# Performance work log

Measured on AMD Instinct MI355X. Metric: run time of the kernel, lower is better.

Reference implementation:

```python
import jax, jax.numpy as jnp
import numpy as np

DIM = 768
HEADS = 12
HEAD_DIM = DIM // HEADS
MAX_LEN = 2048
EPS = 1e-5

def layer_norm(x, w, b):
    mu = jnp.mean(x, axis=-1, keepdims=True)
    var = jnp.var(x, axis=-1, keepdims=True)
    return (x - mu) * jax.lax.rsqrt(var + EPS) * w + b


def setup_inputs() -> dict:
    key = jax.random.key(0)
    ks = jax.random.split(key, 16)
    B, N = 2, 2048
    s = 1.0 / np.sqrt(DIM)
    inp = {
        "visible_features": jax.random.normal(ks[0], (B, N, DIM), jnp.float32),
        "infrared_features": jax.random.normal(ks[1], (B, N, DIM), jnp.float32),
        "wq": jax.random.normal(ks[2], (DIM, DIM), jnp.float32) * s,
        "bq": jnp.zeros((DIM,), jnp.float32),
        "lnq_w": jnp.ones((DIM,), jnp.float32),
        "lnq_b": jnp.zeros((DIM,), jnp.float32),
        "wk": jax.random.normal(ks[3], (DIM, DIM), jnp.float32) * s,
        "bk": jnp.zeros((DIM,), jnp.float32),
        "lnk_w": jnp.ones((DIM,), jnp.float32),
        "lnk_b": jnp.zeros((DIM,), jnp.float32),
        "wv": jax.random.normal(ks[4], (DIM, DIM), jnp.float32) * s,
        "bv": jnp.zeros((DIM,), jnp.float32),
        "lnv_w": jnp.ones((DIM,), jnp.float32),
        "lnv_b": jnp.zeros((DIM,), jnp.float32),
        "pos_emb": jax.random.normal(ks[5], (MAX_LEN, DIM), jnp.float32),
        "wo": jax.random.normal(ks[6], (DIM, DIM), jnp.float32) * s,
        "bo": jnp.zeros((DIM,), jnp.float32),
        "gate_w": jax.random.normal(ks[7], (DIM, 2 * DIM), jnp.float32) * (1.0 / np.sqrt(2 * DIM)),
        "gate_b": jnp.zeros((DIM,), jnp.float32),
        "ln_w": jnp.ones((DIM,), jnp.float32),
        "ln_b": jnp.zeros((DIM,), jnp.float32),
    }
    return inp


def reference(visible_features, infrared_features, wq, bq, lnq_w, lnq_b,
              wk, bk, lnk_w, lnk_b, wv, bv, lnv_w, lnv_b,
              pos_emb, wo, bo, gate_w, gate_b, ln_w, ln_b):
    B, N, _ = visible_features.shape
    scale = HEAD_DIM ** -0.5

    def proj_heads(x, w, b, gw, gb):
        y = layer_norm(x @ w.T + b, gw, gb)  # [B,N,D]
        return y.reshape(B, N, HEADS, HEAD_DIM).transpose(0, 2, 1, 3)  # [B,H,N,d]

    q = proj_heads(infrared_features, wq, bq, lnq_w, lnq_b)
    k = proj_heads(visible_features, wk, bk, lnk_w, lnk_b)
    v = proj_heads(visible_features, wv, bv, lnv_w, lnv_b)

    pos = pos_emb[:N].reshape(1, N, HEADS, HEAD_DIM).transpose(0, 2, 1, 3)  # [1,H,N,d]

    scores = jnp.einsum('bhnd,bhmd->bhnm', q, k) * scale
    scores = scores + jnp.einsum('bhnd,xhmd->bhnm', q, pos)
    attn = jax.nn.softmax(scores, axis=-1)  # dropout is identity in eval

    out = jnp.einsum('bhnm,bhmd->bhnd', attn, v)
    out = out.transpose(0, 2, 1, 3).reshape(B, N, DIM)
    out = out @ wo.T + bo

    gate = jax.nn.sigmoid(jnp.concatenate([visible_features, out], axis=-1) @ gate_w.T + gate_b)
    fused = visible_features * gate + out * (1.0 - gate)
    return layer_norm(fused, ln_w, ln_b)
```

## Files before the change

### kernel.cpp

```cpp
#include <hip/hip_runtime.h>
#include <hip/hip_bf16.h>

#define DIMC 768
#define NSEQ 2048
#define NB 2
#define NH 12
#define HD 64
#define EPSLN 1e-5f
#define LOG2E 1.44269504f

typedef __attribute__((ext_vector_type(8))) short          bf16x8;
typedef __attribute__((ext_vector_type(8))) unsigned short ushort8;
typedef __attribute__((ext_vector_type(4))) unsigned short ushort4v;
typedef __attribute__((ext_vector_type(4))) float          f32x4;
typedef unsigned int u32;

__device__ __forceinline__ unsigned short f2b(float f) {
    union { float f; unsigned u; } x; x.f = f;
    unsigned r = x.u + 0x7fffu + ((x.u >> 16) & 1u);
    return (unsigned short)(r >> 16);
}
__device__ __forceinline__ float b2f(unsigned short v) {
    union { unsigned u; float f; } x; x.u = ((u32)v) << 16; return x.f;
}

#define MFMA16(a, b, c) __builtin_amdgcn_mfma_f32_16x16x32_bf16((a), (b), (c), 0, 0, 0)

__device__ __forceinline__ void gl_lds16(const unsigned short* g, unsigned short* l) {
    __builtin_amdgcn_global_load_lds(
        (const __attribute__((address_space(1))) u32*)(const void*)g,
        (__attribute__((address_space(3))) u32*)(void*)l, 16, 0, 0);
}

#define G_WQ   147456
#define G_MW   442368
#define G_G2   147456
#define G_WO   147456
#define G_VIS  786432
#define G_INF  786432
#define G_BF_TOTAL (G_WQ + G_MW + G_G2 + G_WO + G_VIS + G_INF)
#define G_BIAS 576
#define G_ALL  (G_BF_TOTAL + G_BIAS)

__global__ __launch_bounds__(256)
void cast_all_kernel(const float* __restrict__ wq, const float* __restrict__ wk,
                     const float* __restrict__ wv, const float* __restrict__ gw,
                     const float* __restrict__ wo,
                     const float* __restrict__ bk, const float* __restrict__ bv,
                     const float* __restrict__ gb,
                     const float* __restrict__ vis, const float* __restrict__ inf_,
                     unsigned short* __restrict__ o_wq, unsigned short* __restrict__ o_mw,
                     unsigned short* __restrict__ o_g2, unsigned short* __restrict__ o_wo,
                     unsigned short* __restrict__ o_vis, unsigned short* __restrict__ o_inf,
                     float* __restrict__ o_biasc)
{
    const int g = blockIdx.x * 256 + threadIdx.x;
    if (g >= G_ALL) return;
    if (g >= G_BF_TOTAL) {
        const int e0 = (g - G_BF_TOTAL) * 4;
        float4 r;
        float* pr = (float*)&r;
        #pragma unroll
        for (int t = 0; t < 4; ++t) {
            const int e = e0 + t;
            pr[t] = (e < 768) ? bk[e] : (e < 1536) ? bv[e - 768] : gb[e - 1536];
        }
        *(float4*)&o_biasc[e0] = r;
        return;
    }
    const float* src; unsigned short* dst; int soff, doff = 0;
    int gg = g;
    if (gg < G_WQ) { src = wq; dst = o_wq; soff = gg; doff = gg; }
    else if ((gg -= G_WQ) < G_MW) {
        const int row = gg / 192, c4 = gg % 192;
        dst = o_mw; doff = gg;
        if      (row < 768)  { src = wk; soff = row * 192 + c4; }
        else if (row < 1536) { src = wv; soff = (row - 768) * 192 + c4; }
        else                 { src = gw; soff = (row - 1536) * 384 + c4; }
    }
    else if ((gg -= G_MW) < G_G2) {
        const int row = gg / 192, c4 = gg % 192;
        src = gw; soff = row * 384 + 192 + c4; dst = o_g2; doff = gg;
    }
    else if ((gg -= G_G2) < G_WO)  { src = wo;   dst = o_wo;  soff = gg; doff = gg; }
    else if ((gg -= G_WO) < G_VIS) { src = vis;  dst = o_vis; soff = gg; doff = gg; }
    else { gg -= G_VIS;              src = inf_; dst = o_inf; soff = gg; doff = gg; }
    f32x4 v = ((const f32x4*)src)[soff];
    ushort4v t;
    t[0] = f2b(v[0]); t[1] = f2b(v[1]); t[2] = f2b(v[2]); t[3] = f2b(v[3]);
    ((ushort4v*)dst)[doff] = t;
}

template<int MODE>
__global__ __launch_bounds__(256)
void gemm128(const unsigned short* __restrict__ A,
             const unsigned short* __restrict__ W,
             const float* __restrict__ bias,
             float* __restrict__ Cf,
             unsigned short* __restrict__ Cb)
{
    __shared__ unsigned short As[128 * 64];
    __shared__ unsigned short Bs[128 * 64];
    const int m0 = blockIdx.x * 128, n0 = blockIdx.y * 128;
    const int lane = threadIdx.x & 63, wid = threadIdx.x >> 6;
    const int wm = wid >> 1, wn = wid & 1;
    const int r16 = lane & 15, kg = lane >> 4;
    const int lrow = lane >> 3;
    const int lcol = (lane & 7) * 8;

    f32x4 acc[4][4] = {};

    for (int k0 = 0; k0 < DIMC; k0 += 64) {
        if (k0) __syncthreads();
        #pragma unroll
        for (int i = 0; i < 4; ++i) {
            const int c = wid * 4 + i;
            const int row = c * 8 + lrow;
            gl_lds16(&A[(size_t)(m0 + row) * DIMC + k0 + lcol], &As[c * 512]);
            gl_lds16(&W[(size_t)(n0 + row) * DIMC + k0 + lcol], &Bs[c * 512]);
        }
        __syncthreads();
        #pragma unroll
        for (int ks = 0; ks < 2; ++ks) {
            bf16x8 af[4], bg[4];
            #pragma unroll
            for (int mi = 0; mi < 4; ++mi)
                af[mi] = *(const bf16x8*)&As[(wm * 64 + mi * 16 + r16) * 64 + ks * 32 + kg * 8];
            #pragma unroll
            for (int nj = 0; nj < 4; ++nj)
                bg[nj] = *(const bf16x8*)&Bs[(wn * 64 + nj * 16 + r16) * 64 + ks * 32 + kg * 8];
            __builtin_amdgcn_s_setprio(1);
            #pragma unroll
            for (int mi = 0; mi < 4; ++mi)
                #pragma unroll
                for (int nj = 0; nj < 4; ++nj)
                    acc[mi][nj] = MFMA16(af[mi], bg[nj], acc[mi][nj]);
            __builtin_amdgcn_s_setprio(0);
        }
    }

    #pragma unroll
    for (int mi = 0; mi < 4; ++mi)
    #pragma unroll
    for (int nj = 0; nj < 4; ++nj) {
        const int gr = m0 + wm * 64 + mi * 16 + kg * 4;
        const int gc = n0 + wn * 64 + nj * 16 + r16;
        const float bvl = (MODE == 3) ? 0.f : bias[gc];
        #pragma unroll
        for (int r = 0; r < 4; ++r) {
            const float val = acc[mi][nj][r] + bvl;
            if (MODE == 0) {
                Cf[(size_t)(gr + r) * DIMC + gc] = val;
            } else if (MODE == 1) {
                if (gc < 1536) Cb[(size_t)(gr + r) * 1536 + gc] = f2b(val);
                else           Cf[(size_t)(gr + r) * DIMC + (gc - 1536)] = val;
            } else if (MODE == 2) {
                const size_t idx = (size_t)(gr + r) * DIMC + gc;
                Cf[idx] = val;
                Cb[idx] = f2b(val);
            } else {
                const size_t idx = (size_t)(gr + r) * DIMC + gc;
                Cf[idx] += val;
            }
        }
    }
}

template<int INBF, int MODE>
__global__ __launch_bounds__(256)
void ln_bf16_kernel(const void* __restrict__ Zv,
                    int ld,
                    const float* __restrict__ w,
                    const float* __restrict__ b,
                    const float* __restrict__ pos,
                    unsigned short* __restrict__ out)
{
    const int row = blockIdx.x;
    const int n = row & (NSEQ - 1);
    float x[3];
    float s = 0.f, q = 0.f;
    #pragma unroll
    for (int u = 0; u < 3; ++u) {
        const int j = threadIdx.x + u * 256;
        if (INBF) x[u] = b2f(((const unsigned short*)Zv)[(size_t)row * ld + j]);
        else      x[u] = ((const float*)Zv)[(size_t)row * ld + j];
        s += x[u];
        q += x[u] * x[u];
    }
    #pragma unroll
    for (int off = 32; off > 0; off >>= 1) {
        s += __shfl_down(s, off);
        q += __shfl_down(q, off);
    }
    __shared__ float ls[8];
    const int wv_ = threadIdx.x >> 6;
    if ((threadIdx.x & 63) == 0) { ls[wv_] = s; ls[4 + wv_] = q; }
    __syncthreads();
    if (threadIdx.x == 0) {
        ls[0] = ls[0] + ls[1] + ls[2] + ls[3];
        ls[4] = ls[4] + ls[5] + ls[6] + ls[7];
    }
    __syncthreads();
    const float mu  = ls[0] * (1.f / DIMC);
    const float var = ls[4] * (1.f / DIMC) - mu * mu;
    const float rs  = rsqrtf(var + EPSLN);
    #pragma unroll
    for (int u = 0; u < 3; ++u) {
        const int j = threadIdx.x + u * 256;
        float y = (x[u] - mu) * rs * w[j] + b[j];
        if (MODE == 1) y = y * (0.125f * LOG2E) + pos[(size_t)n * DIMC + j] * LOG2E;
        out[(size_t)row * DIMC + j] = f2b(y);
    }
}

__global__ __launch_bounds__(256)
void attn_bf16_kernel(const unsigned short* __restrict__ Q,
                      const unsigned short* __restrict__ K,
                      const unsigned short* __restrict__ V,
                      unsigned short* __restrict__ O)
{
    __shared__ unsigned short Ks[64][72];
    __shared__ unsigned short Vt[64][72];
    __shared__ unsigned short Ps[4][16][72];

    const int bh = blockIdx.x;
    const int b = bh / NH, h = bh % NH;
    const int n0 = blockIdx.y * 64;
    const int lane = threadIdx.x & 63, w = threadIdx.x >> 6;
    const int r16 = lane & 15, kg = lane >> 4;

    const size_t base = (size_t)b * NSEQ * DIMC + (size_t)h * HD;

    const size_t qoff = base + (size_t)(n0 + w * 16 + r16) * DIMC + kg * 8;
    bf16x8 aq0 = *(const bf16x8*)&Q[qoff];
    bf16x8 aq1 = *(const bf16x8*)&Q[qoff + 32];

    f32x4 o[4] = {};
    float m_run = -1e30f, l_run = 0.f;

    for (int m0 = 0; m0 < NSEQ; m0 += 64) {
        __syncthreads();
        {
            const int kv = threadIdx.x >> 2;
            const int c  = (threadIdx.x & 3) * 16;
            const size_t go = base + (size_t)(m0 + kv) * DIMC + c;
            *(ushort8*)&Ks[kv][c]     = *(const ushort8*)&K[go];
            *(ushort8*)&Ks[kv][c + 8] = *(const ushort8*)&K[go + 8];
        }
        {
            const int kv = threadIdx.x & 63;
            const int dg = (threadIdx.x >> 6) * 16;
            const size_t go = base + (size_t)(m0 + kv) * DIMC + dg;
            #pragma unroll
            for (int i = 0; i < 4; ++i) {
                ushort4v v4 = *(const ushort4v*)&V[go + i * 4];
                Vt[dg + i * 4 + 0][kv] = v4[0];
                Vt[dg + i * 4 + 1][kv] = v4[1];
                Vt[dg + i * 4 + 2][kv] = v4[2];
                Vt[dg + i * 4 + 3][kv] = v4[3];
            }
        }
        __syncthreads();

        f32x4 sv[4];
        #pragma unroll
        for (int f = 0; f < 4; ++f) sv[f] = (f32x4){0.f, 0.f, 0.f, 0.f};
        __builtin_amdgcn_s_setprio(1);
        #pragma unroll
        for (int f = 0; f < 4; ++f) {
            bf16x8 kb0 = *(const bf16x8*)&Ks[f * 16 + r16][kg * 8];
            bf16x8 kb1 = *(const bf16x8*)&Ks[f * 16 + r16][32 + kg * 8];
            sv[f] = MFMA16(kb0, aq0, sv[f]);
            sv[f] = MFMA16(kb1, aq1, sv[f]);
        }
        __builtin_amdgcn_s_setprio(0);

        float mt = sv[0][0];
        #pragma unroll
        for (int f = 0; f < 4; ++f)
            #pragma unroll
            for (int j = 0; j < 4; ++j)
                mt = fmaxf(mt, sv[f][j]);
        mt = fmaxf(mt, __shfl_xor(mt, 16));
        mt = fmaxf(mt, __shfl_xor(mt, 32));
        const float mnew = fmaxf(m_run, mt);
        const float corr = exp2f(m_run - mnew);
        float p[4][4];
        float st = 0.f;
        #pragma unroll
        for (int f = 0; f < 4; ++f)
            #pragma unroll
            for (int j = 0; j < 4; ++j) {
                p[f][j] = exp2f(sv[f][j] - mnew);
                st += p[f][j];
            }
        st += __shfl_xor(st, 16);
        st += __shfl_xor(st, 32);
        l_run = l_run * corr + st;
        m_run = mnew;

        #pragma unroll
        for (int f = 0; f < 4; ++f) {
            u32 w0, w1;
            asm("v_cvt_pk_bf16_f32 %0, %1, %2" : "=v"(w0) : "v"(p[f][0]), "v"(p[f][1]));
            asm("v_cvt_pk_bf16_f32 %0, %1, %2" : "=v"(w1) : "v"(p[f][2]), "v"(p[f][3]));
            *(u32*)&Ps[w][r16][kg * 4 + 16 * f]     = w0;
            *(u32*)&Ps[w][r16][kg * 4 + 2 + 16 * f] = w1;
        }

        #pragma unroll
        for (int jj = 0; jj < 4; ++jj) {
            const float cq = __shfl(corr, kg * 4 + jj);
            o[0][jj] *= cq; o[1][jj] *= cq; o[2][jj] *= cq; o[3][jj] *= cq;
        }

        bf16x8 pa0 = *(const bf16x8*)&Ps[w][r16][kg * 8];
        bf16x8 pa1 = *(const bf16x8*)&Ps[w][r16][32 + kg * 8];
        __builtin_amdgcn_s_setprio(1);
        #pragma unroll
        for (int nj = 0; nj < 4; ++nj) {
            bf16x8 vb0 = *(const bf16x8*)&Vt[nj * 16 + r16][kg * 8];
            bf16x8 vb1 = *(const bf16x8*)&Vt[nj * 16 + r16][32 + kg * 8];
            o[nj] = MFMA16(pa0, vb0, o[nj]);
            o[nj] = MFMA16(pa1, vb1, o[nj]);
        }
        __builtin_amdgcn_s_setprio(0);
    }

    float linv[4];
    #pragma unroll
    for (int jj = 0; jj < 4; ++jj)
        linv[jj] = 1.f / __shfl(l_run, kg * 4 + jj);
    #pragma unroll
    for (int nj = 0; nj < 4; ++nj)
    #pragma unroll
    for (int jj = 0; jj < 4; ++jj) {
        const size_t go = base + (size_t)(n0 + w * 16 + kg * 4 + jj) * DIMC + nj * 16 + r16;
        O[go] = f2b(o[nj][jj] * linv[jj]);
    }
}

__global__ __launch_bounds__(256)
void fuse_ln_kernel(const float* __restrict__ vis,
                    const float* __restrict__ Oc,
                    const float* __restrict__ G,
                    const float* __restrict__ w,
                    const float* __restrict__ b,
                    float* __restrict__ out)
{
    const int row = blockIdx.x;
    float f[3];
    float s = 0.f, q = 0.f;
    #pragma unroll
    for (int u = 0; u < 3; ++u) {
        const size_t idx = (size_t)row * DIMC + threadIdx.x + u * 256;
        const float vv = vis[idx];
        const float oo = Oc[idx];
        const float gg = 1.f / (1.f + __expf(-G[idx]));
        f[u] = vv * gg + oo * (1.f - gg);
        s += f[u];
        q += f[u] * f[u];
    }
    #pragma unroll
    for (int off = 32; off > 0; off >>= 1) {
        s += __shfl_down(s, off);
        q += __shfl_down(q, off);
    }
    __shared__ float ls[8];
    const int wv_ = threadIdx.x >> 6;
    if ((threadIdx.x & 63) == 0) { ls[wv_] = s; ls[4 + wv_] = q; }
    __syncthreads();
    if (threadIdx.x == 0) {
        ls[0] = ls[0] + ls[1] + ls[2] + ls[3];
        ls[4] = ls[4] + ls[5] + ls[6] + ls[7];
    }
    __syncthreads();
    const float mu  = ls[0] * (1.f / DIMC);
    const float var = ls[4] * (1.f / DIMC) - mu * mu;
    const float rs  = rsqrtf(var + EPSLN);
    #pragma unroll
    for (int u = 0; u < 3; ++u) {
        const int j = threadIdx.x + u * 256;
        out[(size_t)row * DIMC + j] = (f[u] - mu) * rs * w[j] + b[j];
    }
}

extern "C" void kernel_launch(void* const* d_in, const int* in_sizes, int n_in,
                              void* d_out, int out_size, void* d_ws, size_t ws_size,
                              hipStream_t stream)
{
    const float* vis  = (const float*)d_in[0];
    const float* inf_ = (const float*)d_in[1];
    const float* wq   = (const float*)d_in[2];
    const float* bq   = (const float*)d_in[3];
    const float* lnqw = (const float*)d_in[4];
    const float* lnqb = (const float*)d_in[5];
    const float* wk   = (const float*)d_in[6];
    const float* bk   = (const float*)d_in[7];
    const float* lnkw = (const float*)d_in[8];
    const float* lnkb = (const float*)d_in[9];
    const float* wv   = (const float*)d_in[10];
    const float* bv   = (const float*)d_in[11];
    const float* lnvw = (const float*)d_in[12];
    const float* lnvb = (const float*)d_in[13];
    const float* pos  = (const float*)d_in[14];
    const float* wo   = (const float*)d_in[15];
    const float* bo   = (const float*)d_in[16];
    const float* gw   = (const float*)d_in[17];
    const float* gb   = (const float*)d_in[18];
    const float* lnw  = (const float*)d_in[19];
    const float* lnb  = (const float*)d_in[20];

    const size_t WEL = 589824;
    const size_t MWEL = 1769472;
    const size_t BUF = (size_t)NB * NSEQ * DIMC;

    unsigned short* p = (unsigned short*)d_ws;
    unsigned short* wq_b  = p;  p += WEL;
    unsigned short* mw_b  = p;  p += MWEL;
    unsigned short* g2_b  = p;  p += WEL;
    unsigned short* wo_b  = p;  p += WEL;
    unsigned short* vis_b = p;  p += BUF;
    unsigned short* inf_b = p;  p += BUF;
    unsigned short* q_b   = p;  p += BUF;
    unsigned short* k_b   = p;  p += BUF;
    unsigned short* v_b   = p;  p += BUF;
    unsigned short* kvpre = p;  p += 2 * BUF;
    float* biasc = (float*)p;

    float* Gd  = (float*)d_out;
    float* Oc  = (float*)k_b;
    unsigned short* oc_b = inf_b;

    dim3 blk(256);

    cast_all_kernel<<<dim3((G_ALL + 255) / 256), blk, 0, stream>>>(
        wq, wk, wv, gw, wo, bk, bv, gb, vis, inf_,
        wq_b, mw_b, g2_b, wo_b, vis_b, inf_b, biasc);

    gemm128<0><<<dim3(32, 6), blk, 0, stream>>>(inf_b, wq_b, bq, Gd, nullptr);
    ln_bf16_kernel<0, 0><<<dim3(4096), blk, 0, stream>>>(Gd, DIMC, lnqw, lnqb, nullptr, q_b);

    gemm128<1><<<dim3(32, 18), blk, 0, stream>>>(vis_b, mw_b, biasc, Gd, kvpre);
    ln_bf16_kernel<1, 1><<<dim3(4096), blk, 0, stream>>>(kvpre, 1536, lnkw, lnkb, pos, k_b);
    ln_bf16_kernel<1, 0><<<dim3(4096), blk, 0, stream>>>(kvpre + DIMC, 1536, lnvw, lnvb, nullptr, v_b);

    attn_bf16_kernel<<<dim3(NB * NH, NSEQ / 64), blk, 0, stream>>>(q_b, k_b, v_b, q_b);

    gemm128<2><<<dim3(32, 6), blk, 0, stream>>>(q_b, wo_b, bo, Oc, oc_b);

    gemm128<3><<<dim3(32, 6), blk, 0, stream>>>(oc_b, g2_b, nullptr, Gd, nullptr);

    fuse_ln_kernel<<<dim3(4096), blk, 0, stream>>>(vis, Oc, Gd, lnw, lnb, (float*)d_out);
}
```

Measured before the change: 326.1 us.

## Double-buffer GEMM tiles, prefetch K/V and defer softmax rescaling in attention

The GEMM kernel moves to 128x64 output tiles with double-buffered LDS staging and explicit vmcnt waits, so global loads overlap the MFMA work and more blocks are launched. The attention kernel now handles 128 query rows per block (32 per wave), which reuses each K/V tile over twice as many queries. It also prefetches the next K/V tile into registers during compute, and skips the running-max update and output rescale while the max grows by at most 8 in log2 units. The tradeoffs are more registers and LDS per block, only 384 attention blocks (fewer than before, which may hurt occupancy), and larger unnormalised exponentials under deferred rescaling.

```diff
diff --git a/kernel.cpp b/kernel.cpp
--- a/kernel.cpp
+++ b/kernel.cpp
@@ -93,58 +93,73 @@
 
 template<int MODE>
 __global__ __launch_bounds__(256)
-void gemm128(const unsigned short* __restrict__ A,
-             const unsigned short* __restrict__ W,
-             const float* __restrict__ bias,
-             float* __restrict__ Cf,
-             unsigned short* __restrict__ Cb)
+void gemm128x64(const unsigned short* __restrict__ A,
+                const unsigned short* __restrict__ W,
+                const float* __restrict__ bias,
+                float* __restrict__ Cf,
+                unsigned short* __restrict__ Cb)
 {
-    __shared__ unsigned short As[128 * 64];
-    __shared__ unsigned short Bs[128 * 64];
-    const int m0 = blockIdx.x * 128, n0 = blockIdx.y * 128;
+    __shared__ unsigned short As[2][128 * 64];
+    __shared__ unsigned short Bs[2][64 * 64];
+    const int m0 = blockIdx.x * 128, n0 = blockIdx.y * 64;
     const int lane = threadIdx.x & 63, wid = threadIdx.x >> 6;
     const int wm = wid >> 1, wn = wid & 1;
     const int r16 = lane & 15, kg = lane >> 4;
-    const int lrow = lane >> 3;
-    const int lcol = (lane & 7) * 8;
-
-    f32x4 acc[4][4] = {};
-
-    for (int k0 = 0; k0 < DIMC; k0 += 64) {
-        if (k0) __syncthreads();
+    const int lr = lane >> 3, lc = (lane & 7) * 8;
+
+    f32x4 acc[4][2] = {};
+
+    auto stage = [&](int k0, int buf) {
         #pragma unroll
         for (int i = 0; i < 4; ++i) {
             const int c = wid * 4 + i;
-            const int row = c * 8 + lrow;
-            gl_lds16(&A[(size_t)(m0 + row) * DIMC + k0 + lcol], &As[c * 512]);
-            gl_lds16(&W[(size_t)(n0 + row) * DIMC + k0 + lcol], &Bs[c * 512]);
-        }
-        __syncthreads();
+            gl_lds16(&A[(size_t)(m0 + c * 8 + lr) * DIMC + k0 + lc], &As[buf][c * 512]);
+        }
+        #pragma unroll
+        for (int i = 0; i < 2; ++i) {
+            const int c = wid * 2 + i;
+            gl_lds16(&W[(size_t)(n0 + c * 8 + lr) * DIMC + k0 + lc], &Bs[buf][c * 512]);
+        }
+    };
+
+    stage(0, 0);
+    for (int t = 0; t < 12; ++t) {
+        const int cur = t & 1;
+        if (t < 11) {
+            stage((t + 1) * 64, cur ^ 1);
+            asm volatile("s_waitcnt vmcnt(6)" ::: "memory");
+        } else {
+            asm volatile("s_waitcnt vmcnt(0)" ::: "memory");
+        }
+        __builtin_amdgcn_s_barrier();
+        __builtin_amdgcn_sched_barrier(0);
         #pragma unroll
         for (int ks = 0; ks < 2; ++ks) {
-            bf16x8 af[4], bg[4];
+            bf16x8 af[4], bg[2];
             #pragma unroll
             for (int mi = 0; mi < 4; ++mi)
-                af[mi] = *(const bf16x8*)&As[(wm * 64 + mi * 16 + r16) * 64 + ks * 32 + kg * 8];
-            #pragma unroll
-            for (int nj = 0; nj < 4; ++nj)
-                bg[nj] = *(const bf16x8*)&Bs[(wn * 64 + nj * 16 + r16) * 64 + ks * 32 + kg * 8];
+                af[mi] = *(const bf16x8*)&As[cur][(wm * 64 + mi * 16 + r16) * 64 + ks * 32 + kg * 8];
+            #pragma unroll
+            for (int nj = 0; nj < 2; ++nj)
+                bg[nj] = *(const bf16x8*)&Bs[cur][(wn * 32 + nj * 16 + r16) * 64 + ks * 32 + kg * 8];
             __builtin_amdgcn_s_setprio(1);
             #pragma unroll
             for (int mi = 0; mi < 4; ++mi)
                 #pragma unroll
-                for (int nj = 0; nj < 4; ++nj)
+                for (int nj = 0; nj < 2; ++nj)
                     acc[mi][nj] = MFMA16(af[mi], bg[nj], acc[mi][nj]);
             __builtin_amdgcn_s_setprio(0);
         }
+        __builtin_amdgcn_sched_barrier(0);
+        __builtin_amdgcn_s_barrier();
     }
 
     #pragma unroll
     for (int mi = 0; mi < 4; ++mi)
     #pragma unroll
-    for (int nj = 0; nj < 4; ++nj) {
+    for (int nj = 0; nj < 2; ++nj) {
         const int gr = m0 + wm * 64 + mi * 16 + kg * 4;
-        const int gc = n0 + wn * 64 + nj * 16 + r16;
+        const int gc = n0 + wn * 32 + nj * 16 + r16;
         const float bvl = (MODE == 3) ? 0.f : bias[gc];
         #pragma unroll
         for (int r = 0; r < 4; ++r) {
@@ -221,123 +236,180 @@
 {
     __shared__ unsigned short Ks[64][72];
     __shared__ unsigned short Vt[64][72];
-    __shared__ unsigned short Ps[4][16][72];
+    __shared__ unsigned short Ps[4][32][72];
 
     const int bh = blockIdx.x;
     const int b = bh / NH, h = bh % NH;
-    const int n0 = blockIdx.y * 64;
+    const int n0 = blockIdx.y * 128;
     const int lane = threadIdx.x & 63, w = threadIdx.x >> 6;
     const int r16 = lane & 15, kg = lane >> 4;
 
     const size_t base = (size_t)b * NSEQ * DIMC + (size_t)h * HD;
 
-    const size_t qoff = base + (size_t)(n0 + w * 16 + r16) * DIMC + kg * 8;
-    bf16x8 aq0 = *(const bf16x8*)&Q[qoff];
-    bf16x8 aq1 = *(const bf16x8*)&Q[qoff + 32];
-
-    f32x4 o[4] = {};
-    float m_run = -1e30f, l_run = 0.f;
+    bf16x8 aq[2][2];
+    #pragma unroll
+    for (int qf = 0; qf < 2; ++qf) {
+        const size_t qo = base + (size_t)(n0 + w * 32 + qf * 16 + r16) * DIMC + kg * 8;
+        aq[qf][0] = *(const bf16x8*)&Q[qo];
+        aq[qf][1] = *(const bf16x8*)&Q[qo + 32];
+    }
+
+    const int krow = threadIdx.x >> 2;
+    const int kcol = (threadIdx.x & 3) * 16;
+    const unsigned short* Kg = K + base + (size_t)krow * DIMC + kcol;
+    const int vrow = threadIdx.x & 63;
+    const int vcol = (threadIdx.x >> 6) * 16;
+    const unsigned short* Vg = V + base + (size_t)vrow * DIMC + vcol;
+
+    f32x4 o[2][4] = {};
+    float m_run[2] = {-1e30f, -1e30f};
+    float l_run[2] = {0.f, 0.f};
+
+    ushort8  kr0 = *(const ushort8*)Kg;
+    ushort8  kr1 = *(const ushort8*)(Kg + 8);
+    ushort4v vr[4];
+    #pragma unroll
+    for (int i = 0; i < 4; ++i) vr[i] = *(const ushort4v*)(Vg + i * 4);
+    *(ushort8*)&Ks[krow][kcol]     = kr0;
+    *(ushort8*)&Ks[krow][kcol + 8] = kr1;
+    #pragma unroll
+    for (int i = 0; i < 4; ++i)
+        #pragma unroll
+        for (int e = 0; e < 4; ++e)
+            Vt[vcol + i * 4 + e][vrow] = vr[i][e];
+    __syncthreads();
 
     for (int m0 = 0; m0 < NSEQ; m0 += 64) {
-        __syncthreads();
-        {
-            const int kv = threadIdx.x >> 2;
-            const int c  = (threadIdx.x & 3) * 16;
-            const size_t go = base + (size_t)(m0 + kv) * DIMC + c;
-            *(ushort8*)&Ks[kv][c]     = *(const ushort8*)&K[go];
-            *(ushort8*)&Ks[kv][c + 8] = *(const ushort8*)&K[go + 8];
-        }
-        {
-            const int kv = threadIdx.x & 63;
-            const int dg = (threadIdx.x >> 6) * 16;
-            const size_t go = base + (size_t)(m0 + kv) * DIMC + dg;
-            #pragma unroll
-            for (int i = 0; i < 4; ++i) {
-                ushort4v v4 = *(const ushort4v*)&V[go + i * 4];
-                Vt[dg + i * 4 + 0][kv] = v4[0];
-                Vt[dg + i * 4 + 1][kv] = v4[1];
-                Vt[dg + i * 4 + 2][kv] = v4[2];
-                Vt[dg + i * 4 + 3][kv] = v4[3];
-            }
-        }
-        __syncthreads();
-
-        f32x4 sv[4];
-        #pragma unroll
-        for (int f = 0; f < 4; ++f) sv[f] = (f32x4){0.f, 0.f, 0.f, 0.f};
+        const bool more = (m0 + 64 < NSEQ);
+        if (more) {
+            const size_t adv = (size_t)(m0 + 64) * DIMC;
+            kr0 = *(const ushort8*)(Kg + adv);
+            kr1 = *(const ushort8*)(Kg + adv + 8);
+            #pragma unroll
+            for (int i = 0; i < 4; ++i) vr[i] = *(const ushort4v*)(Vg + adv + i * 4);
+        }
+        __builtin_amdgcn_sched_barrier(0);
+
+        f32x4 sv[4][2];
+        #pragma unroll
+        for (int f = 0; f < 4; ++f)
+            #pragma unroll
+            for (int qf = 0; qf < 2; ++qf)
+                sv[f][qf] = (f32x4){0.f, 0.f, 0.f, 0.f};
         __builtin_amdgcn_s_setprio(1);
         #pragma unroll
         for (int f = 0; f < 4; ++f) {
             bf16x8 kb0 = *(const bf16x8*)&Ks[f * 16 + r16][kg * 8];
             bf16x8 kb1 = *(const bf16x8*)&Ks[f * 16 + r16][32 + kg * 8];
-            sv[f] = MFMA16(kb0, aq0, sv[f]);
-            sv[f] = MFMA16(kb1, aq1, sv[f]);
+            #pragma unroll
+            for (int qf = 0; qf < 2; ++qf) {
+                sv[f][qf] = MFMA16(kb0, aq[qf][0], sv[f][qf]);
+                sv[f][qf] = MFMA16(kb1, aq[qf][1], sv[f][qf]);
+            }
         }
         __builtin_amdgcn_s_setprio(0);
 
-        float mt = sv[0][0];
-        #pragma unroll
-        for (int f = 0; f < 4; ++f)
-            #pragma unroll
-            for (int j = 0; j < 4; ++j)
-                mt = fmaxf(mt, sv[f][j]);
-        mt = fmaxf(mt, __shfl_xor(mt, 16));
-        mt = fmaxf(mt, __shfl_xor(mt, 32));
-        const float mnew = fmaxf(m_run, mt);
-        const float corr = exp2f(m_run - mnew);
-        float p[4][4];
-        float st = 0.f;
-        #pragma unroll
-        for (int f = 0; f < 4; ++f)
-            #pragma unroll
-            for (int j = 0; j < 4; ++j) {
-                p[f][j] = exp2f(sv[f][j] - mnew);
-                st += p[f][j];
+        float mt[2];
+        #pragma unroll
+        for (int qf = 0; qf < 2; ++qf) {
+            float m = sv[0][qf][0];
+            #pragma unroll
+            for (int f = 0; f < 4; ++f)
+                #pragma unroll
+                for (int j = 0; j < 4; ++j)
+                    m = fmaxf(m, sv[f][qf][j]);
+            m = fmaxf(m, __shfl_xor(m, 16));
+            m = fmaxf(m, __shfl_xor(m, 32));
+            mt[qf] = m;
+        }
+        const float growth = fmaxf(mt[0] - m_run[0], mt[1] - m_run[1]);
+        const bool defer = __all(growth <= 8.0f);
+        float corr[2] = {1.f, 1.f};
+        if (!defer) {
+            #pragma unroll
+            for (int qf = 0; qf < 2; ++qf) {
+                const float mn = fmaxf(m_run[qf], mt[qf]);
+                corr[qf] = exp2f(m_run[qf] - mn);
+                m_run[qf] = mn;
             }
-        st += __shfl_xor(st, 16);
-        st += __shfl_xor(st, 32);
-        l_run = l_run * corr + st;
-        m_run = mnew;
-
-        #pragma unroll
-        for (int f = 0; f < 4; ++f) {
-            u32 w0, w1;
-            asm("v_cvt_pk_bf16_f32 %0, %1, %2" : "=v"(w0) : "v"(p[f][0]), "v"(p[f][1]));
-            asm("v_cvt_pk_bf16_f32 %0, %1, %2" : "=v"(w1) : "v"(p[f][2]), "v"(p[f][3]));
-            *(u32*)&Ps[w][r16][kg * 4 + 16 * f]     = w0;
-            *(u32*)&Ps[w][r16][kg * 4 + 2 + 16 * f] = w1;
-        }
-
+        }
+
+        #pragma unroll
+        for (int qf = 0; qf < 2; ++qf) {
+            float st = 0.f;
+            #pragma unroll
+            for (int f = 0; f < 4; ++f) {
+                float p0 = exp2f(sv[f][qf][0] - m_run[qf]);
+                float p1 = exp2f(sv[f][qf][1] - m_run[qf]);
+                float p2 = exp2f(sv[f][qf][2] - m_run[qf]);
+                float p3 = exp2f(sv[f][qf][3] - m_run[qf]);
+                st += (p0 + p1) + (p2 + p3);
+                u32 w0, w1;
+                asm("v_cvt_pk_bf16_f32 %0, %1, %2" : "=v"(w0) : "v"(p0), "v"(p1));
+                asm("v_cvt_pk_bf16_f32 %0, %1, %2" : "=v"(w1) : "v"(p2), "v"(p3));
+                *(u32*)&Ps[w][qf * 16 + r16][f * 16 + kg * 4]     = w0;
+                *(u32*)&Ps[w][qf * 16 + r16][f * 16 + kg * 4 + 2] = w1;
+            }
+            st += __shfl_xor(st, 16);
+            st += __shfl_xor(st, 32);
+            l_run[qf] = l_run[qf] * corr[qf] + st;
+        }
+
+        if (!defer) {
+            #pragma unroll
+            for (int ri = 0; ri < 2; ++ri)
+                #pragma unroll
+                for (int jj = 0; jj < 4; ++jj) {
+                    const float cq = __shfl(corr[ri], kg * 4 + jj);
+                    #pragma unroll
+                    for (int nj = 0; nj < 4; ++nj) o[ri][nj][jj] *= cq;
+                }
+        }
+
+        __builtin_amdgcn_s_setprio(1);
+        #pragma unroll
+        for (int ri = 0; ri < 2; ++ri) {
+            bf16x8 pa0 = *(const bf16x8*)&Ps[w][ri * 16 + r16][kg * 8];
+            bf16x8 pa1 = *(const bf16x8*)&Ps[w][ri * 16 + r16][32 + kg * 8];
+            #pragma unroll
+            for (int nj = 0; nj < 4; ++nj) {
+                bf16x8 vb0 = *(const bf16x8*)&Vt[nj * 16 + r16][kg * 8];
+                bf16x8 vb1 = *(const bf16x8*)&Vt[nj * 16 + r16][32 + kg * 8];
+                o[ri][nj] = MFMA16(pa0, vb0, o[ri][nj]);
+                o[ri][nj] = MFMA16(pa1, vb1, o[ri][nj]);
+            }
+        }
+        __builtin_amdgcn_s_setprio(0);
+
+        __builtin_amdgcn_s_barrier();
+        __builtin_amdgcn_sched_barrier(0);
+        if (more) {
+            *(ushort8*)&Ks[krow][kcol]     = kr0;
+            *(ushort8*)&Ks[krow][kcol + 8] = kr1;
+            #pragma unroll
+            for (int i = 0; i < 4; ++i)
+                #pragma unroll
+                for (int e = 0; e < 4; ++e)
+                    Vt[vcol + i * 4 + e][vrow] = vr[i][e];
+        }
+        __syncthreads();
+    }
+
+    float rinv[2];
+    rinv[0] = 1.f / l_run[0];
+    rinv[1] = 1.f / l_run[1];
+    #pragma unroll
+    for (int ri = 0; ri < 2; ++ri)
         #pragma unroll
         for (int jj = 0; jj < 4; ++jj) {
-            const float cq = __shfl(corr, kg * 4 + jj);
-            o[0][jj] *= cq; o[1][jj] *= cq; o[2][jj] *= cq; o[3][jj] *= cq;
-        }
-
-        bf16x8 pa0 = *(const bf16x8*)&Ps[w][r16][kg * 8];
-        bf16x8 pa1 = *(const bf16x8*)&Ps[w][r16][32 + kg * 8];
-        __builtin_amdgcn_s_setprio(1);
-        #pragma unroll
-        for (int nj = 0; nj < 4; ++nj) {
-            bf16x8 vb0 = *(const bf16x8*)&Vt[nj * 16 + r16][kg * 8];
-            bf16x8 vb1 = *(const bf16x8*)&Vt[nj * 16 + r16][32 + kg * 8];
-            o[nj] = MFMA16(pa0, vb0, o[nj]);
-            o[nj] = MFMA16(pa1, vb1, o[nj]);
-        }
-        __builtin_amdgcn_s_setprio(0);
-    }
-
-    float linv[4];
-    #pragma unroll
-    for (int jj = 0; jj < 4; ++jj)
-        linv[jj] = 1.f / __shfl(l_run, kg * 4 + jj);
-    #pragma unroll
-    for (int nj = 0; nj < 4; ++nj)
-    #pragma unroll
-    for (int jj = 0; jj < 4; ++jj) {
-        const size_t go = base + (size_t)(n0 + w * 16 + kg * 4 + jj) * DIMC + nj * 16 + r16;
-        O[go] = f2b(o[nj][jj] * linv[jj]);
-    }
+            const float cq = __shfl(rinv[ri], kg * 4 + jj);
+            #pragma unroll
+            for (int nj = 0; nj < 4; ++nj) {
+                const size_t go = base + (size_t)(n0 + w * 32 + ri * 16 + kg * 4 + jj) * DIMC
+                                + nj * 16 + r16;
+                O[go] = f2b(o[ri][nj][jj] * cq);
+            }
+        }
 }
 
 __global__ __launch_bounds__(256)
@@ -438,18 +510,18 @@
         wq, wk, wv, gw, wo, bk, bv, gb, vis, inf_,
         wq_b, mw_b, g2_b, wo_b, vis_b, inf_b, biasc);
 
-    gemm128<0><<<dim3(32, 6), blk, 0, stream>>>(inf_b, wq_b, bq, Gd, nullptr);
+    gemm128x64<0><<<dim3(32, 12), blk, 0, stream>>>(inf_b, wq_b, bq, Gd, nullptr);
     ln_bf16_kernel<0, 0><<<dim3(4096), blk, 0, stream>>>(Gd, DIMC, lnqw, lnqb, nullptr, q_b);
 
-    gemm128<1><<<dim3(32, 18), blk, 0, stream>>>(vis_b, mw_b, biasc, Gd, kvpre);
+    gemm128x64<1><<<dim3(32, 36), blk, 0, stream>>>(vis_b, mw_b, biasc, Gd, kvpre);
     ln_bf16_kernel<1, 1><<<dim3(4096), blk, 0, stream>>>(kvpre, 1536, lnkw, lnkb, pos, k_b);
     ln_bf16_kernel<1, 0><<<dim3(4096), blk, 0, stream>>>(kvpre + DIMC, 1536, lnvw, lnvb, nullptr, v_b);
 
-    attn_bf16_kernel<<<dim3(NB * NH, NSEQ / 64), blk, 0, stream>>>(q_b, k_b, v_b, q_b);
-
-    gemm128<2><<<dim3(32, 6), blk, 0, stream>>>(q_b, wo_b, bo, Oc, oc_b);
-
-    gemm128<3><<<dim3(32, 6), blk, 0, stream>>>(oc_b, g2_b, nullptr, Gd, nullptr);
+    attn_bf16_kernel<<<dim3(NB * NH, NSEQ / 128), blk, 0, stream>>>(q_b, k_b, v_b, q_b);
+
+    gemm128x64<2><<<dim3(32, 12), blk, 0, stream>>>(q_b, wo_b, bo, Oc, oc_b);
+
+    gemm128x64<3><<<dim3(32, 12), blk, 0, stream>>>(oc_b, g2_b, nullptr, Gd, nullptr);
 
     fuse_ln_kernel<<<dim3(4096), blk, 0, stream>>>(vis, Oc, Gd, lnw, lnb, (float*)d_out);
 }
```

Measured after the change: 314.0 us. 1.04x faster.
